# Kernel tuning notes

Measured on AMD Instinct MI355X. Metric: run time of the kernel, lower is better.

Reference implementation:

```python
import jax, jax.numpy as jnp
import numpy as np

N = 1024
D = 128          # node_dim
NUM_LAYERS = 3
H_CLS = 128      # edge classifier hidden


def setup_inputs() -> dict:
    key = jax.random.key(0)
    ks = jax.random.split(key, 20)
    s_in = 1.0 / np.sqrt(3.0)
    s_d = 1.0 / np.sqrt(D)
    s_2d = 1.0 / np.sqrt(2 * D)
    s_h = 1.0 / np.sqrt(H_CLS)
    inp = {
        "node_features": jax.random.uniform(ks[0], (N, 3), jnp.float32),
        "adj_matrix": jax.random.uniform(ks[1], (N, N), jnp.float32),
        "edge_weights": jax.random.normal(ks[2], (N, N, 1), jnp.float32),
        # node embedding Linear(3, D)
        "W_embed": jax.random.uniform(ks[3], (3, D), jnp.float32, -s_in, s_in),
        "b_embed": jax.random.uniform(ks[4], (D,), jnp.float32, -s_in, s_in),
        # stacked GCN layer params, [L, ...]
        "Wu": jax.random.uniform(ks[5], (NUM_LAYERS, D, D), jnp.float32, -s_d, s_d),
        "bu": jax.random.uniform(ks[6], (NUM_LAYERS, D), jnp.float32, -s_d, s_d),
        "Wv": jax.random.uniform(ks[7], (NUM_LAYERS, D, D), jnp.float32, -s_d, s_d),
        "bv": jax.random.uniform(ks[8], (NUM_LAYERS, D), jnp.float32, -s_d, s_d),
        "Wg": jax.random.uniform(ks[9], (NUM_LAYERS, 2 * D, D), jnp.float32, -s_2d, s_2d),
        "bg": jax.random.uniform(ks[10], (NUM_LAYERS, D), jnp.float32, -s_2d, s_2d),
        # edge classifier: Linear(2D, 128) -> ReLU -> Linear(128, 1)
        "Wc1": jax.random.uniform(ks[11], (2 * D, H_CLS), jnp.float32, -s_2d, s_2d),
        "bc1": jax.random.uniform(ks[12], (H_CLS,), jnp.float32, -s_2d, s_2d),
        "Wc2": jax.random.uniform(ks[13], (H_CLS, 1), jnp.float32, -s_h, s_h),
        "bc2": jax.random.uniform(ks[14], (1,), jnp.float32, -s_h, s_h),
    }
    return inp


def reference(node_features, adj_matrix, edge_weights,
              W_embed, b_embed, Wu, bu, Wv, bv, Wg, bg,
              Wc1, bc1, Wc2, bc2):
    h = node_features @ W_embed + b_embed                       # [N, D]
    for l in range(NUM_LAYERS):
        u = h @ Wu[l] + bu[l]                                   # [N, D]
        v = h @ Wv[l] + bv[l]                                   # [N, D]
        agg = adj_matrix @ v                                    # [N, D]
        # gate Linear(2D, D) on cat([u, agg]) == u @ Wg[:D] + agg @ Wg[D:]
        gate = jax.nn.sigmoid(u @ Wg[l, :D] + agg @ Wg[l, D:] + bg[l])
        h = jax.nn.relu(h + gate * agg)
    # edge classifier: cat([h_i, h_j]) @ Wc1 == (h @ Wc1[:D])[i] + (h @ Wc1[D:])[j]
    hi = h @ Wc1[:D]                                            # [N, H]
    hj = h @ Wc1[D:]                                            # [N, H]
    hidden = jax.nn.relu(hi[:, None, :] + hj[None, :, :] + bc1) # [N, N, H]
    logits = jnp.einsum('ijh,h->ij', hidden, Wc2[:, 0]) + bc2[0]  # [N, N]
    loss = jnp.mean(jnp.square(logits * adj_matrix - edge_weights[..., 0]))
    return logits, loss
```

## Files before the change

kernel.cpp:

```cpp
#include <hip/hip_runtime.h>

#define NN 1024
#define DD 128

typedef __attribute__((ext_vector_type(8))) __bf16 bf16x8;
typedef __attribute__((ext_vector_type(4))) float f32x4;

__device__ __forceinline__ float us2f(unsigned short b) { return __uint_as_float(((unsigned)b) << 16); }
__device__ __forceinline__ unsigned short f2bf(float f) {
    unsigned x = __float_as_uint(f);
    return (unsigned short)((x + 0x7fffu + ((x >> 16) & 1u)) >> 16);
}

__global__ __launch_bounds__(256) void k_prep_embuv(
    const float* __restrict__ adj, unsigned short* __restrict__ aH, unsigned short* __restrict__ aL,
    const float* __restrict__ nf, const float* __restrict__ We, const float* __restrict__ be,
    const float* __restrict__ Wu, const float* __restrict__ bu,
    const float* __restrict__ Wv, const float* __restrict__ bv,
    float* __restrict__ h, float* __restrict__ u,
    unsigned short* __restrict__ vTh, unsigned short* __restrict__ vTl,
    float* __restrict__ lossAcc, unsigned* __restrict__ counter)
{
    __shared__ float hS[4][DD];
    int b = blockIdx.x, tid = threadIdx.x;
    if (b < 1024) {
        int idx = (b * 256 + tid) * 4;
        float4 a = *(const float4*)(adj + idx);
        ushort4 hv, lv;
        hv.x = f2bf(a.x); lv.x = f2bf(a.x - us2f(hv.x));
        hv.y = f2bf(a.y); lv.y = f2bf(a.y - us2f(hv.y));
        hv.z = f2bf(a.z); lv.z = f2bf(a.z - us2f(hv.z));
        hv.w = f2bf(a.w); lv.w = f2bf(a.w - us2f(hv.w));
        *(ushort4*)(aH + idx) = hv;
        *(ushort4*)(aL + idx) = lv;
        if (b == 0 && tid == 0) { *lossAcc = 0.f; *counter = 0u; }
        return;
    }
    int m0 = (b - 1024) * 4;
    int d = tid & 127, half = tid >> 7;
    float hr[4];
#pragma unroll
    for (int r = 0; r < 4; ++r) {
        float a = be[d];
#pragma unroll
        for (int k = 0; k < 3; ++k) a = fmaf(nf[(m0 + r) * 3 + k], We[k * DD + d], a);
        hr[r] = a;
    }
    if (half == 0) {
#pragma unroll
        for (int r = 0; r < 4; ++r) { h[(m0 + r) * DD + d] = hr[r]; hS[r][d] = hr[r]; }
    }
    __syncthreads();
    const float* W = half ? Wv : Wu;
    float acc[4] = {0.f, 0.f, 0.f, 0.f};
#pragma unroll 4
    for (int k4 = 0; k4 < DD; k4 += 4) {
        f32x4 h0 = *(const f32x4*)&hS[0][k4];
        f32x4 h1 = *(const f32x4*)&hS[1][k4];
        f32x4 h2 = *(const f32x4*)&hS[2][k4];
        f32x4 h3 = *(const f32x4*)&hS[3][k4];
#pragma unroll
        for (int kk = 0; kk < 4; ++kk) {
            float w = W[(k4 + kk) * DD + d];
            acc[0] = fmaf(h0[kk], w, acc[0]);
            acc[1] = fmaf(h1[kk], w, acc[1]);
            acc[2] = fmaf(h2[kk], w, acc[2]);
            acc[3] = fmaf(h3[kk], w, acc[3]);
        }
    }
    if (half == 0) {
        float bb = bu[d];
#pragma unroll
        for (int r = 0; r < 4; ++r) u[(m0 + r) * DD + d] = acc[r] + bb;
    } else {
        float bb = bv[d];
        float v0 = acc[0] + bb, v1 = acc[1] + bb, v2 = acc[2] + bb, v3 = acc[3] + bb;
        ushort4 hv, lv;
        hv.x = f2bf(v0); lv.x = f2bf(v0 - us2f(hv.x));
        hv.y = f2bf(v1); lv.y = f2bf(v1 - us2f(hv.y));
        hv.z = f2bf(v2); lv.z = f2bf(v2 - us2f(hv.z));
        hv.w = f2bf(v3); lv.w = f2bf(v3 - us2f(hv.w));
        *(ushort4*)(vTh + d * NN + m0) = hv;
        *(ushort4*)(vTl + d * NN + m0) = lv;
    }
}

__global__ __launch_bounds__(256) void k_agg(
    const unsigned short* __restrict__ adjH, const unsigned short* __restrict__ adjL,
    const unsigned short* __restrict__ vTh, const unsigned short* __restrict__ vTl,
    float* __restrict__ P)
{
    int tid = threadIdx.x, lane = tid & 63, w = tid >> 6;
    int b = blockIdx.x;
    int nt = b >> 7;
    int mt = (b >> 1) & 63;
    int kc = ((b & 1) << 2) | w;
    int m = lane & 15, quad = lane >> 4;
    int k0 = kc * 128 + quad * 8;
    const unsigned short* ah = adjH + (size_t)(mt * 16 + m) * NN + k0;
    const unsigned short* al = adjL + (size_t)(mt * 16 + m) * NN + k0;
    const unsigned short* bh = vTh + (size_t)(nt * 16 + m) * NN + k0;
    const unsigned short* bl = vTl + (size_t)(nt * 16 + m) * NN + k0;
    f32x4 acc = {0.f, 0.f, 0.f, 0.f};
#pragma unroll
    for (int kt = 0; kt < 4; ++kt) {
        bf16x8 aH = *(const bf16x8*)(ah + kt * 32);
        bf16x8 aL = *(const bf16x8*)(al + kt * 32);
        bf16x8 bH = *(const bf16x8*)(bh + kt * 32);
        bf16x8 bL = *(const bf16x8*)(bl + kt * 32);
        acc = __builtin_amdgcn_mfma_f32_16x16x32_bf16(aH, bH, acc, 0, 0, 0);
        acc = __builtin_amdgcn_mfma_f32_16x16x32_bf16(aH, bL, acc, 0, 0, 0);
        acc = __builtin_amdgcn_mfma_f32_16x16x32_bf16(aL, bH, acc, 0, 0, 0);
    }
    float* Pk = P + (size_t)kc * (NN * DD);
    int row0 = mt * 16 + quad * 4;
    int col = nt * 16 + m;
#pragma unroll
    for (int r = 0; r < 4; ++r) Pk[(row0 + r) * DD + col] = acc[r];
}

__global__ __launch_bounds__(256) void k_gateuv(
    const float* __restrict__ P, float* __restrict__ u, float* __restrict__ h,
    const float* __restrict__ Wg, const float* __restrict__ bg,
    const float* __restrict__ Wun, const float* __restrict__ bun,
    const float* __restrict__ Wvn, const float* __restrict__ bvn,
    unsigned short* __restrict__ vTh, unsigned short* __restrict__ vTl)
{
    __shared__ float uS[4][DD], aS[4][DD], hS[4][DD];
    int tid = threadIdx.x;
    int m0 = blockIdx.x * 4;
    int d = tid & 127, half = tid >> 7;
#pragma unroll
    for (int e = tid; e < 512; e += 256) {
        int r = e >> 7, dd = e & 127;
        int idx = (m0 + r) * DD + dd;
        float s = 0.f;
#pragma unroll
        for (int c = 0; c < 8; ++c) s += P[(size_t)c * (NN * DD) + idx];
        aS[r][dd] = s;
        uS[r][dd] = u[idx];
    }
    __syncthreads();
    const float* WA = Wg;
    const float* WB = Wg + DD * DD;
    int r0 = half * 2;
    float acc[2] = {0.f, 0.f};
#pragma unroll 4
    for (int k4 = 0; k4 < DD; k4 += 4) {
        f32x4 u0 = *(const f32x4*)&uS[r0][k4];
        f32x4 u1 = *(const f32x4*)&uS[r0 + 1][k4];
        f32x4 a0 = *(const f32x4*)&aS[r0][k4];
        f32x4 a1 = *(const f32x4*)&aS[r0 + 1][k4];
#pragma unroll
        for (int kk = 0; kk < 4; ++kk) {
            float wa = WA[(k4 + kk) * DD + d];
            float wb = WB[(k4 + kk) * DD + d];
            acc[0] = fmaf(u0[kk], wa, fmaf(a0[kk], wb, acc[0]));
            acc[1] = fmaf(u1[kk], wa, fmaf(a1[kk], wb, acc[1]));
        }
    }
    float bgd = bg[d];
#pragma unroll
    for (int rr = 0; rr < 2; ++rr) {
        int r = r0 + rr;
        float g = 1.f / (1.f + __expf(-(acc[rr] + bgd)));
        float nh = fmaf(g, aS[r][d], h[(m0 + r) * DD + d]);
        nh = nh > 0.f ? nh : 0.f;
        h[(m0 + r) * DD + d] = nh;
        hS[r][d] = nh;
    }
    __syncthreads();
    const float* W = half ? Wvn : Wun;
    float av[4] = {0.f, 0.f, 0.f, 0.f};
#pragma unroll 4
    for (int k4 = 0; k4 < DD; k4 += 4) {
        f32x4 h0 = *(const f32x4*)&hS[0][k4];
        f32x4 h1 = *(const f32x4*)&hS[1][k4];
        f32x4 h2 = *(const f32x4*)&hS[2][k4];
        f32x4 h3 = *(const f32x4*)&hS[3][k4];
#pragma unroll
        for (int kk = 0; kk < 4; ++kk) {
            float w = W[(k4 + kk) * DD + d];
            av[0] = fmaf(h0[kk], w, av[0]);
            av[1] = fmaf(h1[kk], w, av[1]);
            av[2] = fmaf(h2[kk], w, av[2]);
            av[3] = fmaf(h3[kk], w, av[3]);
        }
    }
    if (half == 0) {
        float bb = bun[d];
#pragma unroll
        for (int r = 0; r < 4; ++r) u[(m0 + r) * DD + d] = av[r] + bb;
    } else {
        float bb = bvn[d];
        float v0 = av[0] + bb, v1 = av[1] + bb, v2 = av[2] + bb, v3 = av[3] + bb;
        ushort4 hv, lv;
        hv.x = f2bf(v0); lv.x = f2bf(v0 - us2f(hv.x));
        hv.y = f2bf(v1); lv.y = f2bf(v1 - us2f(hv.y));
        hv.z = f2bf(v2); lv.z = f2bf(v2 - us2f(hv.z));
        hv.w = f2bf(v3); lv.w = f2bf(v3 - us2f(hv.w));
        *(ushort4*)(vTh + d * NN + m0) = hv;
        *(ushort4*)(vTl + d * NN + m0) = lv;
    }
}

__global__ __launch_bounds__(256) void k_gatecls(
    const float* __restrict__ P, float* __restrict__ u, float* __restrict__ h,
    const float* __restrict__ Wg, const float* __restrict__ bg,
    const float* __restrict__ Wc1, const float* __restrict__ bc1, const float* __restrict__ Wc2,
    float* __restrict__ hi, float* __restrict__ hj,
    float* __restrict__ S1, float* __restrict__ S2)
{
    __shared__ float uS[4][DD], aS[4][DD], hS[4][DD];
    __shared__ float sred[2][4];
    int tid = threadIdx.x;
    int m0 = blockIdx.x * 4;
    int d = tid & 127, half = tid >> 7;
    if (tid < 8) sred[tid >> 2][tid & 3] = 0.f;
#pragma unroll
    for (int e = tid; e < 512; e += 256) {
        int r = e >> 7, dd = e & 127;
        int idx = (m0 + r) * DD + dd;
        float s = 0.f;
#pragma unroll
        for (int c = 0; c < 8; ++c) s += P[(size_t)c * (NN * DD) + idx];
        aS[r][dd] = s;
        uS[r][dd] = u[idx];
    }
    __syncthreads();
    const float* WA = Wg;
    const float* WB = Wg + DD * DD;
    int r0 = half * 2;
    float acc[2] = {0.f, 0.f};
#pragma unroll 4
    for (int k4 = 0; k4 < DD; k4 += 4) {
        f32x4 u0 = *(const f32x4*)&uS[r0][k4];
        f32x4 u1 = *(const f32x4*)&uS[r0 + 1][k4];
        f32x4 a0 = *(const f32x4*)&aS[r0][k4];
        f32x4 a1 = *(const f32x4*)&aS[r0 + 1][k4];
#pragma unroll
        for (int kk = 0; kk < 4; ++kk) {
            float wa = WA[(k4 + kk) * DD + d];
            float wb = WB[(k4 + kk) * DD + d];
            acc[0] = fmaf(u0[kk], wa, fmaf(a0[kk], wb, acc[0]));
            acc[1] = fmaf(u1[kk], wa, fmaf(a1[kk], wb, acc[1]));
        }
    }
    float bgd = bg[d];
#pragma unroll
    for (int rr = 0; rr < 2; ++rr) {
        int r = r0 + rr;
        float g = 1.f / (1.f + __expf(-(acc[rr] + bgd)));
        float nh = fmaf(g, aS[r][d], h[(m0 + r) * DD + d]);
        nh = nh > 0.f ? nh : 0.f;
        hS[r][d] = nh;
    }
    __syncthreads();
    const float* W = Wc1 + (half ? DD * DD : 0);
    float av[4] = {0.f, 0.f, 0.f, 0.f};
#pragma unroll 4
    for (int k4 = 0; k4 < DD; k4 += 4) {
        f32x4 h0 = *(const f32x4*)&hS[0][k4];
        f32x4 h1 = *(const f32x4*)&hS[1][k4];
        f32x4 h2 = *(const f32x4*)&hS[2][k4];
        f32x4 h3 = *(const f32x4*)&hS[3][k4];
#pragma unroll
        for (int kk = 0; kk < 4; ++kk) {
            float w = W[(k4 + kk) * DD + d];
            av[0] = fmaf(h0[kk], w, av[0]);
            av[1] = fmaf(h1[kk], w, av[1]);
            av[2] = fmaf(h2[kk], w, av[2]);
            av[3] = fmaf(h3[kk], w, av[3]);
        }
    }
    float wv = Wc2[d];
    float bcv = half ? 0.f : bc1[d];
    float* out = half ? hj : hi;
    int lane = tid & 63;
#pragma unroll
    for (int r = 0; r < 4; ++r) {
        float val = av[r] + bcv;
        out[(m0 + r) * DD + d] = val;
        float p = val * wv;
#pragma unroll
        for (int off = 32; off; off >>= 1) p += __shfl_down(p, off);
        if (lane == 0) atomicAdd(&sred[half][r], p);
    }
    __syncthreads();
    if (tid < 4) S1[m0 + tid] = sred[0][tid];
    else if (tid < 8) S2[m0 + tid - 4] = sred[1][tid - 4];
}

__global__ __launch_bounds__(256) void k_edge(
    const float* __restrict__ hi, const float* __restrict__ hj,
    const float* __restrict__ S1, const float* __restrict__ S2,
    const float* __restrict__ Wc2, const float* __restrict__ bc2,
    const float* __restrict__ adj, const float* __restrict__ ew,
    float* __restrict__ outL, float* __restrict__ lossAcc, unsigned* __restrict__ counter)
{
    __shared__ float hiT[128][68];
    __shared__ float hjT[128][68];
    __shared__ float wS[128];
    __shared__ float lred;
    int tid = threadIdx.x;
    int i0 = (blockIdx.x >> 4) * 64, j0 = (blockIdx.x & 15) * 64;
    if (tid == 0) lred = 0.f;
    if (tid < 128) wS[tid] = Wc2[tid];
    for (int e = tid; e < 64 * 128; e += 256) {
        int r = e >> 7, hh = e & 127;
        hiT[hh][r] = hi[(i0 + r) * DD + hh];
        hjT[hh][r] = hj[(j0 + r) * DD + hh];
    }
    __syncthreads();
    int tx = tid & 15, ty = tid >> 4;
    float acc[4][4] = {};
#pragma unroll 4
    for (int hh = 0; hh < 128; ++hh) {
        f32x4 a = *(const f32x4*)&hiT[hh][ty * 4];
        f32x4 b = *(const f32x4*)&hjT[hh][tx * 4];
        float w = wS[hh];
#pragma unroll
        for (int p = 0; p < 4; ++p)
#pragma unroll
            for (int q = 0; q < 4; ++q) {
                float x = a[p] + b[q];
                acc[p][q] = fmaf(fabsf(x), w, acc[p][q]);
            }
    }
    float bcv = bc2[0];
    float ls = 0.f;
#pragma unroll
    for (int p = 0; p < 4; ++p) {
        int i = i0 + ty * 4 + p;
        float s1 = S1[i];
        int jb = j0 + tx * 4;
        f32x4 s2 = *(const f32x4*)(S2 + jb);
        f32x4 lg;
#pragma unroll
        for (int q = 0; q < 4; ++q)
            lg[q] = fmaf(0.5f, acc[p][q] + s1 + s2[q], bcv);
        *(f32x4*)(outL + (size_t)i * NN + jb) = lg;
        f32x4 a4 = *(const f32x4*)(adj + (size_t)i * NN + jb);
        f32x4 e4 = *(const f32x4*)(ew + (size_t)i * NN + jb);
#pragma unroll
        for (int q = 0; q < 4; ++q) {
            float t = fmaf(lg[q], a4[q], -e4[q]);
            ls = fmaf(t, t, ls);
        }
    }
#pragma unroll
    for (int off = 32; off; off >>= 1) ls += __shfl_down(ls, off);
    if ((tid & 63) == 0) atomicAdd(&lred, ls);
    __syncthreads();
    if (tid == 0) {
        atomicAdd(lossAcc, lred);
        __threadfence();
        unsigned old = atomicAdd(counter, 1u);
        if (old == 255u) {
            __threadfence();
            outL[(size_t)NN * NN] = (*(volatile float*)lossAcc) * (1.f / (1024.f * 1024.f));
        }
    }
}

extern "C" void kernel_launch(void* const* d_in, const int* in_sizes, int n_in,
                              void* d_out, int out_size, void* d_ws, size_t ws_size,
                              hipStream_t stream)
{
    const float* nf  = (const float*)d_in[0];
    const float* adj = (const float*)d_in[1];
    const float* ew  = (const float*)d_in[2];
    const float* We  = (const float*)d_in[3];
    const float* be  = (const float*)d_in[4];
    const float* Wu  = (const float*)d_in[5];
    const float* bu  = (const float*)d_in[6];
    const float* Wv  = (const float*)d_in[7];
    const float* bv  = (const float*)d_in[8];
    const float* Wg  = (const float*)d_in[9];
    const float* bg  = (const float*)d_in[10];
    const float* Wc1 = (const float*)d_in[11];
    const float* bc1 = (const float*)d_in[12];
    const float* Wc2 = (const float*)d_in[13];
    const float* bc2 = (const float*)d_in[14];

    float* ws = (float*)d_ws;
    float* h   = ws;
    float* u   = ws + 131072;
    unsigned short* vTh = (unsigned short*)(ws + 262144);
    unsigned short* vTl = (unsigned short*)(ws + 327680);
    float* P   = ws + 393216;
    unsigned short* adjH = (unsigned short*)(ws + 1441792);
    unsigned short* adjL = (unsigned short*)(ws + 1966080);
    float* hi  = ws + 2490368;
    float* hj  = ws + 2621440;
    float* S1  = ws + 2752512;
    float* S2  = ws + 2753536;
    float* lossAcc = ws + 2754560;
    unsigned* counter = (unsigned*)(ws + 2754561);

    k_prep_embuv<<<1280, 256, 0, stream>>>(adj, adjH, adjL, nf, We, be,
                                           Wu, bu, Wv, bv, h, u, vTh, vTl, lossAcc, counter);
    for (int l = 0; l < 3; ++l) {
        k_agg<<<1024, 256, 0, stream>>>(adjH, adjL, vTh, vTl, P);
        if (l < 2)
            k_gateuv<<<256, 256, 0, stream>>>(P, u, h, Wg + l * 32768, bg + l * 128,
                                              Wu + (l + 1) * 16384, bu + (l + 1) * 128,
                                              Wv + (l + 1) * 16384, bv + (l + 1) * 128,
                                              vTh, vTl);
        else
            k_gatecls<<<256, 256, 0, stream>>>(P, u, h, Wg + 2 * 32768, bg + 2 * 128,
                                               Wc1, bc1, Wc2, hi, hj, S1, S2);
    }
    k_edge<<<256, 256, 0, stream>>>(hi, hj, S1, S2, Wc2, bc2, adj, ew,
                                    (float*)d_out, lossAcc, counter);
}
```

Measured before the change: 188.2 us.

## Fuse all stages into one persistent kernel with software grid barriers

Replaces the eight separate kernel launches (prep, three agg/gate pairs, edge) with a single persistent kernel of 256 blocks. The stages are separated by a custom grid barrier built on atomic counters spread over 16 slots. A memset zeroes the loss accumulator and the barrier counters. The aim is to remove launch gaps and inter-kernel drain between small stages. In exchange, the agg stage now runs 1024 tiles on only 256 blocks with lower parallelism, and the kernel depends on all blocks being co-resident.

New measurement: 558.3 us. +196.7%, slower.

```diff
diff --git a/kernel.cpp b/kernel.cpp
--- a/kernel.cpp
+++ b/kernel.cpp
@@ -2,6 +2,7 @@
 
 #define NN 1024
 #define DD 128
+#define NBLK 256
 
 typedef __attribute__((ext_vector_type(8))) __bf16 bf16x8;
 typedef __attribute__((ext_vector_type(4))) float f32x4;
@@ -12,355 +13,303 @@
     return (unsigned short)((x + 0x7fffu + ((x >> 16) & 1u)) >> 16);
 }
 
-__global__ __launch_bounds__(256) void k_prep_embuv(
-    const float* __restrict__ adj, unsigned short* __restrict__ aH, unsigned short* __restrict__ aL,
+__device__ __forceinline__ void gridbar(unsigned* cnt, unsigned epoch) {
+    __syncthreads();
+    __threadfence();
+    int tid = threadIdx.x;
+    if (tid == 0)
+        __hip_atomic_fetch_add(&cnt[(blockIdx.x & 15) << 5], 1u,
+                               __ATOMIC_RELEASE, __HIP_MEMORY_SCOPE_AGENT);
+    if (tid < 16) {
+        unsigned tgt = epoch << 4;
+        while (__hip_atomic_load(&cnt[tid << 5],
+                                 __ATOMIC_ACQUIRE, __HIP_MEMORY_SCOPE_AGENT) < tgt)
+            __builtin_amdgcn_s_sleep(1);
+    }
+    __threadfence();
+    __syncthreads();
+}
+
+__global__ __launch_bounds__(256) void k_fused(
+    const float* __restrict__ adj, const float* __restrict__ ew,
     const float* __restrict__ nf, const float* __restrict__ We, const float* __restrict__ be,
     const float* __restrict__ Wu, const float* __restrict__ bu,
     const float* __restrict__ Wv, const float* __restrict__ bv,
+    const float* __restrict__ Wg, const float* __restrict__ bg,
+    const float* __restrict__ Wc1, const float* __restrict__ bc1,
+    const float* __restrict__ Wc2, const float* __restrict__ bc2,
     float* __restrict__ h, float* __restrict__ u,
     unsigned short* __restrict__ vTh, unsigned short* __restrict__ vTl,
-    float* __restrict__ lossAcc, unsigned* __restrict__ counter)
+    float* __restrict__ P,
+    unsigned short* __restrict__ adjH, unsigned short* __restrict__ adjL,
+    float* __restrict__ hi, float* __restrict__ hj,
+    float* __restrict__ S1, float* __restrict__ S2,
+    float* __restrict__ lossAcc, unsigned* __restrict__ barCnt,
+    float* __restrict__ outL)
 {
-    __shared__ float hS[4][DD];
-    int b = blockIdx.x, tid = threadIdx.x;
-    if (b < 1024) {
-        int idx = (b * 256 + tid) * 4;
-        float4 a = *(const float4*)(adj + idx);
-        ushort4 hv, lv;
-        hv.x = f2bf(a.x); lv.x = f2bf(a.x - us2f(hv.x));
-        hv.y = f2bf(a.y); lv.y = f2bf(a.y - us2f(hv.y));
-        hv.z = f2bf(a.z); lv.z = f2bf(a.z - us2f(hv.z));
-        hv.w = f2bf(a.w); lv.w = f2bf(a.w - us2f(hv.w));
-        *(ushort4*)(aH + idx) = hv;
-        *(ushort4*)(aL + idx) = lv;
-        if (b == 0 && tid == 0) { *lossAcc = 0.f; *counter = 0u; }
-        return;
+    __shared__ union SMem {
+        float hS4[4][DD];
+        struct { float uS[4][DD], aS[4][DD], hS[4][DD], sred[2][4]; } g;
+        struct { float hiT[128][68], hjT[128][68], wS[128], lred; } e;
+    } sm;
+
+    int tid = threadIdx.x;
+    int bx = blockIdx.x;
+    int d = tid & 127, half = tid >> 7;
+    unsigned ep = 0;
+
+    for (int t = bx; t < 1280; t += NBLK) {
+        if (t < 1024) {
+            int idx = (t * 256 + tid) * 4;
+            float4 a = *(const float4*)(adj + idx);
+            ushort4 hv, lv;
+            hv.x = f2bf(a.x); lv.x = f2bf(a.x - us2f(hv.x));
+            hv.y = f2bf(a.y); lv.y = f2bf(a.y - us2f(hv.y));
+            hv.z = f2bf(a.z); lv.z = f2bf(a.z - us2f(hv.z));
+            hv.w = f2bf(a.w); lv.w = f2bf(a.w - us2f(hv.w));
+            *(ushort4*)(adjH + idx) = hv;
+            *(ushort4*)(adjL + idx) = lv;
+        } else {
+            int m0 = (t - 1024) * 4;
+            float hr[4];
+#pragma unroll
+            for (int r = 0; r < 4; ++r) {
+                float a = be[d];
+#pragma unroll
+                for (int k = 0; k < 3; ++k) a = fmaf(nf[(m0 + r) * 3 + k], We[k * DD + d], a);
+                hr[r] = a;
+            }
+            if (half == 0) {
+#pragma unroll
+                for (int r = 0; r < 4; ++r) { h[(m0 + r) * DD + d] = hr[r]; sm.hS4[r][d] = hr[r]; }
+            }
+            __syncthreads();
+            const float* W = half ? Wv : Wu;
+            float acc[4] = {0.f, 0.f, 0.f, 0.f};
+#pragma unroll 4
+            for (int k4 = 0; k4 < DD; k4 += 4) {
+                f32x4 h0 = *(const f32x4*)&sm.hS4[0][k4];
+                f32x4 h1 = *(const f32x4*)&sm.hS4[1][k4];
+                f32x4 h2 = *(const f32x4*)&sm.hS4[2][k4];
+                f32x4 h3 = *(const f32x4*)&sm.hS4[3][k4];
+#pragma unroll
+                for (int kk = 0; kk < 4; ++kk) {
+                    float w = W[(k4 + kk) * DD + d];
+                    acc[0] = fmaf(h0[kk], w, acc[0]);
+                    acc[1] = fmaf(h1[kk], w, acc[1]);
+                    acc[2] = fmaf(h2[kk], w, acc[2]);
+                    acc[3] = fmaf(h3[kk], w, acc[3]);
+                }
+            }
+            if (half == 0) {
+                float bb = bu[d];
+#pragma unroll
+                for (int r = 0; r < 4; ++r) u[(m0 + r) * DD + d] = acc[r] + bb;
+            } else {
+                float bb = bv[d];
+                float v0 = acc[0] + bb, v1 = acc[1] + bb, v2 = acc[2] + bb, v3 = acc[3] + bb;
+                ushort4 hv, lv;
+                hv.x = f2bf(v0); lv.x = f2bf(v0 - us2f(hv.x));
+                hv.y = f2bf(v1); lv.y = f2bf(v1 - us2f(hv.y));
+                hv.z = f2bf(v2); lv.z = f2bf(v2 - us2f(hv.z));
+                hv.w = f2bf(v3); lv.w = f2bf(v3 - us2f(hv.w));
+                *(ushort4*)(vTh + d * NN + m0) = hv;
+                *(ushort4*)(vTl + d * NN + m0) = lv;
+            }
+        }
     }
-    int m0 = (b - 1024) * 4;
-    int d = tid & 127, half = tid >> 7;
-    float hr[4];
-#pragma unroll
-    for (int r = 0; r < 4; ++r) {
-        float a = be[d];
-#pragma unroll
-        for (int k = 0; k < 3; ++k) a = fmaf(nf[(m0 + r) * 3 + k], We[k * DD + d], a);
-        hr[r] = a;
+    gridbar(barCnt, ++ep);
+
+    for (int l = 0; l < 3; ++l) {
+        {
+            int lane = tid & 63, w = tid >> 6;
+            for (int t = bx; t < 1024; t += NBLK) {
+                int nt = t >> 7;
+                int mt = (t >> 1) & 63;
+                int kc = ((t & 1) << 2) | w;
+                int m = lane & 15, quad = lane >> 4;
+                int k0 = kc * 128 + quad * 8;
+                const unsigned short* ah = adjH + (size_t)(mt * 16 + m) * NN + k0;
+                const unsigned short* al = adjL + (size_t)(mt * 16 + m) * NN + k0;
+                const unsigned short* bh = vTh + (size_t)(nt * 16 + m) * NN + k0;
+                const unsigned short* bl = vTl + (size_t)(nt * 16 + m) * NN + k0;
+                f32x4 acc = {0.f, 0.f, 0.f, 0.f};
+#pragma unroll
+                for (int kt = 0; kt < 4; ++kt) {
+                    bf16x8 aH = *(const bf16x8*)(ah + kt * 32);
+                    bf16x8 aL = *(const bf16x8*)(al + kt * 32);
+                    bf16x8 bH = *(const bf16x8*)(bh + kt * 32);
+                    bf16x8 bL = *(const bf16x8*)(bl + kt * 32);
+                    acc = __builtin_amdgcn_mfma_f32_16x16x32_bf16(aH, bH, acc, 0, 0, 0);
+                    acc = __builtin_amdgcn_mfma_f32_16x16x32_bf16(aH, bL, acc, 0, 0, 0);
+                    acc = __builtin_amdgcn_mfma_f32_16x16x32_bf16(aL, bH, acc, 0, 0, 0);
+                }
+                float* Pk = P + (size_t)kc * (NN * DD);
+                int row0 = mt * 16 + quad * 4;
+                int col = nt * 16 + m;
+#pragma unroll
+                for (int r = 0; r < 4; ++r) Pk[(row0 + r) * DD + col] = acc[r];
+            }
+        }
+        gridbar(barCnt, ++ep);
+
+        {
+            int m0 = bx * 4;
+#pragma unroll
+            for (int e2 = tid; e2 < 512; e2 += 256) {
+                int r = e2 >> 7, dd = e2 & 127;
+                int idx = (m0 + r) * DD + dd;
+                float s = 0.f;
+#pragma unroll
+                for (int c = 0; c < 8; ++c) s += P[(size_t)c * (NN * DD) + idx];
+                sm.g.aS[r][dd] = s;
+                sm.g.uS[r][dd] = u[idx];
+            }
+            if (l == 2 && tid < 8) sm.g.sred[tid >> 2][tid & 3] = 0.f;
+            __syncthreads();
+            const float* WA = Wg + l * 32768;
+            const float* WB = WA + DD * DD;
+            int r0 = half * 2;
+            float acc[2] = {0.f, 0.f};
+#pragma unroll 4
+            for (int k4 = 0; k4 < DD; k4 += 4) {
+                f32x4 u0 = *(const f32x4*)&sm.g.uS[r0][k4];
+                f32x4 u1 = *(const f32x4*)&sm.g.uS[r0 + 1][k4];
+                f32x4 a0 = *(const f32x4*)&sm.g.aS[r0][k4];
+                f32x4 a1 = *(const f32x4*)&sm.g.aS[r0 + 1][k4];
+#pragma unroll
+                for (int kk = 0; kk < 4; ++kk) {
+                    float wa = WA[(k4 + kk) * DD + d];
+                    float wb = WB[(k4 + kk) * DD + d];
+                    acc[0] = fmaf(u0[kk], wa, fmaf(a0[kk], wb, acc[0]));
+                    acc[1] = fmaf(u1[kk], wa, fmaf(a1[kk], wb, acc[1]));
+                }
+            }
+            float bgd = bg[l * 128 + d];
+#pragma unroll
+            for (int rr = 0; rr < 2; ++rr) {
+                int r = r0 + rr;
+                float g = 1.f / (1.f + __expf(-(acc[rr] + bgd)));
+                float nh = fmaf(g, sm.g.aS[r][d], h[(m0 + r) * DD + d]);
+                nh = nh > 0.f ? nh : 0.f;
+                if (l < 2) h[(m0 + r) * DD + d] = nh;
+                sm.g.hS[r][d] = nh;
+            }
+            __syncthreads();
+            const float* W2 = (l < 2) ? ((half ? Wv : Wu) + (l + 1) * 16384)
+                                      : (Wc1 + (half ? DD * DD : 0));
+            float av[4] = {0.f, 0.f, 0.f, 0.f};
+#pragma unroll 4
+            for (int k4 = 0; k4 < DD; k4 += 4) {
+                f32x4 h0 = *(const f32x4*)&sm.g.hS[0][k4];
+                f32x4 h1 = *(const f32x4*)&sm.g.hS[1][k4];
+                f32x4 h2 = *(const f32x4*)&sm.g.hS[2][k4];
+                f32x4 h3 = *(const f32x4*)&sm.g.hS[3][k4];
+#pragma unroll
+                for (int kk = 0; kk < 4; ++kk) {
+                    float w = W2[(k4 + kk) * DD + d];
+                    av[0] = fmaf(h0[kk], w, av[0]);
+                    av[1] = fmaf(h1[kk], w, av[1]);
+                    av[2] = fmaf(h2[kk], w, av[2]);
+                    av[3] = fmaf(h3[kk], w, av[3]);
+                }
+            }
+            if (l < 2) {
+                if (half == 0) {
+                    float bb = bu[(l + 1) * 128 + d];
+#pragma unroll
+                    for (int r = 0; r < 4; ++r) u[(m0 + r) * DD + d] = av[r] + bb;
+                } else {
+                    float bb = bv[(l + 1) * 128 + d];
+                    float v0 = av[0] + bb, v1 = av[1] + bb, v2 = av[2] + bb, v3 = av[3] + bb;
+                    ushort4 hv, lv;
+                    hv.x = f2bf(v0); lv.x = f2bf(v0 - us2f(hv.x));
+                    hv.y = f2bf(v1); lv.y = f2bf(v1 - us2f(hv.y));
+                    hv.z = f2bf(v2); lv.z = f2bf(v2 - us2f(hv.z));
+                    hv.w = f2bf(v3); lv.w = f2bf(v3 - us2f(hv.w));
+                    *(ushort4*)(vTh + d * NN + m0) = hv;
+                    *(ushort4*)(vTl + d * NN + m0) = lv;
+                }
+            } else {
+                float wv = Wc2[d];
+                float bcv = half ? 0.f : bc1[d];
+                float* out2 = half ? hj : hi;
+                int lane = tid & 63;
+#pragma unroll
+                for (int r = 0; r < 4; ++r) {
+                    float val = av[r] + bcv;
+                    out2[(m0 + r) * DD + d] = val;
+                    float p = val * wv;
+#pragma unroll
+                    for (int off = 32; off; off >>= 1) p += __shfl_down(p, off);
+                    if (lane == 0) atomicAdd(&sm.g.sred[half][r], p);
+                }
+                __syncthreads();
+                if (tid < 4) S1[m0 + tid] = sm.g.sred[0][tid];
+                else if (tid < 8) S2[m0 + tid - 4] = sm.g.sred[1][tid - 4];
+            }
+        }
+        gridbar(barCnt, ++ep);
     }
-    if (half == 0) {
-#pragma unroll
-        for (int r = 0; r < 4; ++r) { h[(m0 + r) * DD + d] = hr[r]; hS[r][d] = hr[r]; }
+
+    {
+        int i0 = (bx >> 4) * 64, j0 = (bx & 15) * 64;
+        if (tid == 0) sm.e.lred = 0.f;
+        if (tid < 128) sm.e.wS[tid] = Wc2[tid];
+        for (int e2 = tid; e2 < 64 * 128; e2 += 256) {
+            int r = e2 >> 7, hh = e2 & 127;
+            sm.e.hiT[hh][r] = hi[(i0 + r) * DD + hh];
+            sm.e.hjT[hh][r] = hj[(j0 + r) * DD + hh];
+        }
+        __syncthreads();
+        int tx = tid & 15, ty = tid >> 4;
+        float acc[4][4] = {};
+#pragma unroll 4
+        for (int hh = 0; hh < 128; ++hh) {
+            f32x4 a = *(const f32x4*)&sm.e.hiT[hh][ty * 4];
+            f32x4 b = *(const f32x4*)&sm.e.hjT[hh][tx * 4];
+            float w = sm.e.wS[hh];
+#pragma unroll
+            for (int p = 0; p < 4; ++p)
+#pragma unroll
+                for (int q = 0; q < 4; ++q) {
+                    float x = a[p] + b[q];
+                    acc[p][q] = fmaf(fabsf(x), w, acc[p][q]);
+                }
+        }
+        float bcv = bc2[0];
+        float ls = 0.f;
+#pragma unroll
+        for (int p = 0; p < 4; ++p) {
+            int i = i0 + ty * 4 + p;
+            float s1 = S1[i];
+            int jb = j0 + tx * 4;
+            f32x4 s2 = *(const f32x4*)(S2 + jb);
+            f32x4 lg;
+#pragma unroll
+            for (int q = 0; q < 4; ++q)
+                lg[q] = fmaf(0.5f, acc[p][q] + s1 + s2[q], bcv);
+            *(f32x4*)(outL + (size_t)i * NN + jb) = lg;
+            f32x4 a4 = *(const f32x4*)(adj + (size_t)i * NN + jb);
+            f32x4 e4 = *(const f32x4*)(ew + (size_t)i * NN + jb);
+#pragma unroll
+            for (int q = 0; q < 4; ++q) {
+                float t = fmaf(lg[q], a4[q], -e4[q]);
+                ls = fmaf(t, t, ls);
+            }
+        }
+#pragma unroll
+        for (int off = 32; off; off >>= 1) ls += __shfl_down(ls, off);
+        if ((tid & 63) == 0) atomicAdd(&sm.e.lred, ls);
+        __syncthreads();
+        if (tid == 0) atomicAdd(lossAcc, sm.e.lred);
     }
-    __syncthreads();
-    const float* W = half ? Wv : Wu;
-    float acc[4] = {0.f, 0.f, 0.f, 0.f};
-#pragma unroll 4
-    for (int k4 = 0; k4 < DD; k4 += 4) {
-        f32x4 h0 = *(const f32x4*)&hS[0][k4];
-        f32x4 h1 = *(const f32x4*)&hS[1][k4];
-        f32x4 h2 = *(const f32x4*)&hS[2][k4];
-        f32x4 h3 = *(const f32x4*)&hS[3][k4];
-#pragma unroll
-        for (int kk = 0; kk < 4; ++kk) {
-            float w = W[(k4 + kk) * DD + d];
-            acc[0] = fmaf(h0[kk], w, acc[0]);
-            acc[1] = fmaf(h1[kk], w, acc[1]);
-            acc[2] = fmaf(h2[kk], w, acc[2]);
-            acc[3] = fmaf(h3[kk], w, acc[3]);
-        }
-    }
-    if (half == 0) {
-        float bb = bu[d];
-#pragma unroll
-        for (int r = 0; r < 4; ++r) u[(m0 + r) * DD + d] = acc[r] + bb;
-    } else {
-        float bb = bv[d];
-        float v0 = acc[0] + bb, v1 = acc[1] + bb, v2 = acc[2] + bb, v3 = acc[3] + bb;
-        ushort4 hv, lv;
-        hv.x = f2bf(v0); lv.x = f2bf(v0 - us2f(hv.x));
-        hv.y = f2bf(v1); lv.y = f2bf(v1 - us2f(hv.y));
-        hv.z = f2bf(v2); lv.z = f2bf(v2 - us2f(hv.z));
-        hv.w = f2bf(v3); lv.w = f2bf(v3 - us2f(hv.w));
-        *(ushort4*)(vTh + d * NN + m0) = hv;
-        *(ushort4*)(vTl + d * NN + m0) = lv;
-    }
-}
-
-__global__ __launch_bounds__(256) void k_agg(
-    const unsigned short* __restrict__ adjH, const unsigned short* __restrict__ adjL,
-    const unsigned short* __restrict__ vTh, const unsigned short* __restrict__ vTl,
-    float* __restrict__ P)
-{
-    int tid = threadIdx.x, lane = tid & 63, w = tid >> 6;
-    int b = blockIdx.x;
-    int nt = b >> 7;
-    int mt = (b >> 1) & 63;
-    int kc = ((b & 1) << 2) | w;
-    int m = lane & 15, quad = lane >> 4;
-    int k0 = kc * 128 + quad * 8;
-    const unsigned short* ah = adjH + (size_t)(mt * 16 + m) * NN + k0;
-    const unsigned short* al = adjL + (size_t)(mt * 16 + m) * NN + k0;
-    const unsigned short* bh = vTh + (size_t)(nt * 16 + m) * NN + k0;
-    const unsigned short* bl = vTl + (size_t)(nt * 16 + m) * NN + k0;
-    f32x4 acc = {0.f, 0.f, 0.f, 0.f};
-#pragma unroll
-    for (int kt = 0; kt < 4; ++kt) {
-        bf16x8 aH = *(const bf16x8*)(ah + kt * 32);
-        bf16x8 aL = *(const bf16x8*)(al + kt * 32);
-        bf16x8 bH = *(const bf16x8*)(bh + kt * 32);
-        bf16x8 bL = *(const bf16x8*)(bl + kt * 32);
-        acc = __builtin_amdgcn_mfma_f32_16x16x32_bf16(aH, bH, acc, 0, 0, 0);
-        acc = __builtin_amdgcn_mfma_f32_16x16x32_bf16(aH, bL, acc, 0, 0, 0);
-        acc = __builtin_amdgcn_mfma_f32_16x16x32_bf16(aL, bH, acc, 0, 0, 0);
-    }
-    float* Pk = P + (size_t)kc * (NN * DD);
-    int row0 = mt * 16 + quad * 4;
-    int col = nt * 16 + m;
-#pragma unroll
-    for (int r = 0; r < 4; ++r) Pk[(row0 + r) * DD + col] = acc[r];
-}
-
-__global__ __launch_bounds__(256) void k_gateuv(
-    const float* __restrict__ P, float* __restrict__ u, float* __restrict__ h,
-    const float* __restrict__ Wg, const float* __restrict__ bg,
-    const float* __restrict__ Wun, const float* __restrict__ bun,
-    const float* __restrict__ Wvn, const float* __restrict__ bvn,
-    unsigned short* __restrict__ vTh, unsigned short* __restrict__ vTl)
-{
-    __shared__ float uS[4][DD], aS[4][DD], hS[4][DD];
-    int tid = threadIdx.x;
-    int m0 = blockIdx.x * 4;
-    int d = tid & 127, half = tid >> 7;
-#pragma unroll
-    for (int e = tid; e < 512; e += 256) {
-        int r = e >> 7, dd = e & 127;
-        int idx = (m0 + r) * DD + dd;
-        float s = 0.f;
-#pragma unroll
-        for (int c = 0; c < 8; ++c) s += P[(size_t)c * (NN * DD) + idx];
-        aS[r][dd] = s;
-        uS[r][dd] = u[idx];
-    }
-    __syncthreads();
-    const float* WA = Wg;
-    const float* WB = Wg + DD * DD;
-    int r0 = half * 2;
-    float acc[2] = {0.f, 0.f};
-#pragma unroll 4
-    for (int k4 = 0; k4 < DD; k4 += 4) {
-        f32x4 u0 = *(const f32x4*)&uS[r0][k4];
-        f32x4 u1 = *(const f32x4*)&uS[r0 + 1][k4];
-        f32x4 a0 = *(const f32x4*)&aS[r0][k4];
-        f32x4 a1 = *(const f32x4*)&aS[r0 + 1][k4];
-#pragma unroll
-        for (int kk = 0; kk < 4; ++kk) {
-            float wa = WA[(k4 + kk) * DD + d];
-            float wb = WB[(k4 + kk) * DD + d];
-            acc[0] = fmaf(u0[kk], wa, fmaf(a0[kk], wb, acc[0]));
-            acc[1] = fmaf(u1[kk], wa, fmaf(a1[kk], wb, acc[1]));
-        }
-    }
-    float bgd = bg[d];
-#pragma unroll
-    for (int rr = 0; rr < 2; ++rr) {
-        int r = r0 + rr;
-        float g = 1.f / (1.f + __expf(-(acc[rr] + bgd)));
-        float nh = fmaf(g, aS[r][d], h[(m0 + r) * DD + d]);
-        nh = nh > 0.f ? nh : 0.f;
-        h[(m0 + r) * DD + d] = nh;
-        hS[r][d] = nh;
-    }
-    __syncthreads();
-    const float* W = half ? Wvn : Wun;
-    float av[4] = {0.f, 0.f, 0.f, 0.f};
-#pragma unroll 4
-    for (int k4 = 0; k4 < DD; k4 += 4) {
-        f32x4 h0 = *(const f32x4*)&hS[0][k4];
-        f32x4 h1 = *(const f32x4*)&hS[1][k4];
-        f32x4 h2 = *(const f32x4*)&hS[2][k4];
-        f32x4 h3 = *(const f32x4*)&hS[3][k4];
-#pragma unroll
-        for (int kk = 0; kk < 4; ++kk) {
-            float w = W[(k4 + kk) * DD + d];
-            av[0] = fmaf(h0[kk], w, av[0]);
-            av[1] = fmaf(h1[kk], w, av[1]);
-            av[2] = fmaf(h2[kk], w, av[2]);
-            av[3] = fmaf(h3[kk], w, av[3]);
-        }
-    }
-    if (half == 0) {
-        float bb = bun[d];
-#pragma unroll
-        for (int r = 0; r < 4; ++r) u[(m0 + r) * DD + d] = av[r] + bb;
-    } else {
-        float bb = bvn[d];
-        float v0 = av[0] + bb, v1 = av[1] + bb, v2 = av[2] + bb, v3 = av[3] + bb;
-        ushort4 hv, lv;
-        hv.x = f2bf(v0); lv.x = f2bf(v0 - us2f(hv.x));
-        hv.y = f2bf(v1); lv.y = f2bf(v1 - us2f(hv.y));
-        hv.z = f2bf(v2); lv.z = f2bf(v2 - us2f(hv.z));
-        hv.w = f2bf(v3); lv.w = f2bf(v3 - us2f(hv.w));
-        *(ushort4*)(vTh + d * NN + m0) = hv;
-        *(ushort4*)(vTl + d * NN + m0) = lv;
-    }
-}
-
-__global__ __launch_bounds__(256) void k_gatecls(
-    const float* __restrict__ P, float* __restrict__ u, float* __restrict__ h,
-    const float* __restrict__ Wg, const float* __restrict__ bg,
-    const float* __restrict__ Wc1, const float* __restrict__ bc1, const float* __restrict__ Wc2,
-    float* __restrict__ hi, float* __restrict__ hj,
-    float* __restrict__ S1, float* __restrict__ S2)
-{
-    __shared__ float uS[4][DD], aS[4][DD], hS[4][DD];
-    __shared__ float sred[2][4];
-    int tid = threadIdx.x;
-    int m0 = blockIdx.x * 4;
-    int d = tid & 127, half = tid >> 7;
-    if (tid < 8) sred[tid >> 2][tid & 3] = 0.f;
-#pragma unroll
-    for (int e = tid; e < 512; e += 256) {
-        int r = e >> 7, dd = e & 127;
-        int idx = (m0 + r) * DD + dd;
-        float s = 0.f;
-#pragma unroll
-        for (int c = 0; c < 8; ++c) s += P[(size_t)c * (NN * DD) + idx];
-        aS[r][dd] = s;
-        uS[r][dd] = u[idx];
-    }
-    __syncthreads();
-    const float* WA = Wg;
-    const float* WB = Wg + DD * DD;
-    int r0 = half * 2;
-    float acc[2] = {0.f, 0.f};
-#pragma unroll 4
-    for (int k4 = 0; k4 < DD; k4 += 4) {
-        f32x4 u0 = *(const f32x4*)&uS[r0][k4];
-        f32x4 u1 = *(const f32x4*)&uS[r0 + 1][k4];
-        f32x4 a0 = *(const f32x4*)&aS[r0][k4];
-        f32x4 a1 = *(const f32x4*)&aS[r0 + 1][k4];
-#pragma unroll
-        for (int kk = 0; kk < 4; ++kk) {
-            float wa = WA[(k4 + kk) * DD + d];
-            float wb = WB[(k4 + kk) * DD + d];
-            acc[0] = fmaf(u0[kk], wa, fmaf(a0[kk], wb, acc[0]));
-            acc[1] = fmaf(u1[kk], wa, fmaf(a1[kk], wb, acc[1]));
-        }
-    }
-    float bgd = bg[d];
-#pragma unroll
-    for (int rr = 0; rr < 2; ++rr) {
-        int r = r0 + rr;
-        float g = 1.f / (1.f + __expf(-(acc[rr] + bgd)));
-        float nh = fmaf(g, aS[r][d], h[(m0 + r) * DD + d]);
-        nh = nh > 0.f ? nh : 0.f;
-        hS[r][d] = nh;
-    }
-    __syncthreads();
-    const float* W = Wc1 + (half ? DD * DD : 0);
-    float av[4] = {0.f, 0.f, 0.f, 0.f};
-#pragma unroll 4
-    for (int k4 = 0; k4 < DD; k4 += 4) {
-        f32x4 h0 = *(const f32x4*)&hS[0][k4];
-        f32x4 h1 = *(const f32x4*)&hS[1][k4];
-        f32x4 h2 = *(const f32x4*)&hS[2][k4];
-        f32x4 h3 = *(const f32x4*)&hS[3][k4];
-#pragma unroll
-        for (int kk = 0; kk < 4; ++kk) {
-            float w = W[(k4 + kk) * DD + d];
-            av[0] = fmaf(h0[kk], w, av[0]);
-            av[1] = fmaf(h1[kk], w, av[1]);
-            av[2] = fmaf(h2[kk], w, av[2]);
-            av[3] = fmaf(h3[kk], w, av[3]);
-        }
-    }
-    float wv = Wc2[d];
-    float bcv = half ? 0.f : bc1[d];
-    float* out = half ? hj : hi;
-    int lane = tid & 63;
-#pragma unroll
-    for (int r = 0; r < 4; ++r) {
-        float val = av[r] + bcv;
-        out[(m0 + r) * DD + d] = val;
-        float p = val * wv;
-#pragma unroll
-        for (int off = 32; off; off >>= 1) p += __shfl_down(p, off);
-        if (lane == 0) atomicAdd(&sred[half][r], p);
-    }
-    __syncthreads();
-    if (tid < 4) S1[m0 + tid] = sred[0][tid];
-    else if (tid < 8) S2[m0 + tid - 4] = sred[1][tid - 4];
-}
-
-__global__ __launch_bounds__(256) void k_edge(
-    const float* __restrict__ hi, const float* __restrict__ hj,
-    const float* __restrict__ S1, const float* __restrict__ S2,
-    const float* __restrict__ Wc2, const float* __restrict__ bc2,
-    const float* __restrict__ adj, const float* __restrict__ ew,
-    float* __restrict__ outL, float* __restrict__ lossAcc, unsigned* __restrict__ counter)
-{
-    __shared__ float hiT[128][68];
-    __shared__ float hjT[128][68];
-    __shared__ float wS[128];
-    __shared__ float lred;
-    int tid = threadIdx.x;
-    int i0 = (blockIdx.x >> 4) * 64, j0 = (blockIdx.x & 15) * 64;
-    if (tid == 0) lred = 0.f;
-    if (tid < 128) wS[tid] = Wc2[tid];
-    for (int e = tid; e < 64 * 128; e += 256) {
-        int r = e >> 7, hh = e & 127;
-        hiT[hh][r] = hi[(i0 + r) * DD + hh];
-        hjT[hh][r] = hj[(j0 + r) * DD + hh];
-    }
-    __syncthreads();
-    int tx = tid & 15, ty = tid >> 4;
-    float acc[4][4] = {};
-#pragma unroll 4
-    for (int hh = 0; hh < 128; ++hh) {
-        f32x4 a = *(const f32x4*)&hiT[hh][ty * 4];
-        f32x4 b = *(const f32x4*)&hjT[hh][tx * 4];
-        float w = wS[hh];
-#pragma unroll
-        for (int p = 0; p < 4; ++p)
-#pragma unroll
-            for (int q = 0; q < 4; ++q) {
-                float x = a[p] + b[q];
-                acc[p][q] = fmaf(fabsf(x), w, acc[p][q]);
-            }
-    }
-    float bcv = bc2[0];
-    float ls = 0.f;
-#pragma unroll
-    for (int p = 0; p < 4; ++p) {
-        int i = i0 + ty * 4 + p;
-        float s1 = S1[i];
-        int jb = j0 + tx * 4;
-        f32x4 s2 = *(const f32x4*)(S2 + jb);
-        f32x4 lg;
-#pragma unroll
-        for (int q = 0; q < 4; ++q)
-            lg[q] = fmaf(0.5f, acc[p][q] + s1 + s2[q], bcv);
-        *(f32x4*)(outL + (size_t)i * NN + jb) = lg;
-        f32x4 a4 = *(const f32x4*)(adj + (size_t)i * NN + jb);
-        f32x4 e4 = *(const f32x4*)(ew + (size_t)i * NN + jb);
-#pragma unroll
-        for (int q = 0; q < 4; ++q) {
-            float t = fmaf(lg[q], a4[q], -e4[q]);
-            ls = fmaf(t, t, ls);
-        }
-    }
-#pragma unroll
-    for (int off = 32; off; off >>= 1) ls += __shfl_down(ls, off);
-    if ((tid & 63) == 0) atomicAdd(&lred, ls);
-    __syncthreads();
-    if (tid == 0) {
-        atomicAdd(lossAcc, lred);
-        __threadfence();
-        unsigned old = atomicAdd(counter, 1u);
-        if (old == 255u) {
-            __threadfence();
-            outL[(size_t)NN * NN] = (*(volatile float*)lossAcc) * (1.f / (1024.f * 1024.f));
-        }
-    }
+    gridbar(barCnt, ++ep);
+
+    if (bx == 0 && tid == 0)
+        outL[(size_t)NN * NN] =
+            __hip_atomic_load(lossAcc, __ATOMIC_RELAXED, __HIP_MEMORY_SCOPE_AGENT) *
+            (1.f / (1024.f * 1024.f));
 }
 
 extern "C" void kernel_launch(void* const* d_in, const int* in_sizes, int n_in,
@@ -396,21 +345,11 @@
     float* S1  = ws + 2752512;
     float* S2  = ws + 2753536;
     float* lossAcc = ws + 2754560;
-    unsigned* counter = (unsigned*)(ws + 2754561);
-
-    k_prep_embuv<<<1280, 256, 0, stream>>>(adj, adjH, adjL, nf, We, be,
-                                           Wu, bu, Wv, bv, h, u, vTh, vTl, lossAcc, counter);
-    for (int l = 0; l < 3; ++l) {
-        k_agg<<<1024, 256, 0, stream>>>(adjH, adjL, vTh, vTl, P);
-        if (l < 2)
-            k_gateuv<<<256, 256, 0, stream>>>(P, u, h, Wg + l * 32768, bg + l * 128,
-                                              Wu + (l + 1) * 16384, bu + (l + 1) * 128,
-                                              Wv + (l + 1) * 16384, bv + (l + 1) * 128,
-                                              vTh, vTl);
-        else
-            k_gatecls<<<256, 256, 0, stream>>>(P, u, h, Wg + 2 * 32768, bg + 2 * 128,
-                                               Wc1, bc1, Wc2, hi, hj, S1, S2);
-    }
-    k_edge<<<256, 256, 0, stream>>>(hi, hj, S1, S2, Wc2, bc2, adj, ew,
-                                    (float*)d_out, lossAcc, counter);
+    unsigned* barCnt = (unsigned*)(ws + 2754592);
+
+    hipMemsetAsync((void*)lossAcc, 0, 2176, stream);
+    k_fused<<<NBLK, 256, 0, stream>>>(adj, ew, nf, We, be, Wu, bu, Wv, bv, Wg, bg,
+                                      Wc1, bc1, Wc2, bc2, h, u, vTh, vTl, P,
+                                      adjH, adjL, hi, hj, S1, S2,
+                                      lossAcc, barCnt, (float*)d_out);
 }
```
